# Performance work log

Hardware: AMD Instinct MI355X
Metric: run time of the kernel (lower is better)

## Reference

```python
import jax, jax.numpy as jnp
import numpy as np

D_MODEL = 768
NUM_HEADS = 12
D_K = D_MODEL // NUM_HEADS


def setup_inputs() -> dict:
    key = jax.random.key(0)
    ks = jax.random.split(key, 11)
    B, L = 1, 4096
    s = 1.0 / np.sqrt(D_MODEL)
    return {
        "q": jax.random.normal(ks[0], (B, L, D_MODEL), jnp.float32),
        "k": jax.random.normal(ks[1], (B, L, D_MODEL), jnp.float32),
        "v": jax.random.normal(ks[2], (B, L, D_MODEL), jnp.float32),
        "Wq": jax.random.normal(ks[3], (D_MODEL, D_MODEL), jnp.float32) * s,
        "bq": jax.random.normal(ks[4], (D_MODEL,), jnp.float32) * s,
        "Wk": jax.random.normal(ks[5], (D_MODEL, D_MODEL), jnp.float32) * s,
        "bk": jax.random.normal(ks[6], (D_MODEL,), jnp.float32) * s,
        "Wv": jax.random.normal(ks[7], (D_MODEL, D_MODEL), jnp.float32) * s,
        "bv": jax.random.normal(ks[8], (D_MODEL,), jnp.float32) * s,
        "Wo": jax.random.normal(ks[9], (D_MODEL, D_MODEL), jnp.float32) * s,
        "bo": jax.random.normal(ks[10], (D_MODEL,), jnp.float32) * s,
    }


def reference(q, k, v, Wq, bq, Wk, bk, Wv, bv, Wo, bo):
    B, L, _ = q.shape
    # linear projections (torch Linear: x @ W.T + b)
    qp = q @ Wq.T + bq
    kp = k @ Wk.T + bk
    vp = v @ Wv.T + bv
    # split heads: (B, H, L, d_k)
    def split(x):
        return x.reshape(B, L, NUM_HEADS, D_K).transpose(0, 2, 1, 3)
    qh, kh, vh = split(qp), split(kp), split(vp)
    scale = 1.0 / jnp.sqrt(jnp.asarray(D_K, qh.dtype))
    scores = jnp.einsum("bhqd,bhkd->bhqk", qh, kh) * scale  # (B,H,L,L)
    weights = jax.nn.softmax(scores, axis=-1)
    out = jnp.einsum("bhqk,bhkd->bhqd", weights, vh)
    out = out.transpose(0, 2, 1, 3).reshape(B, L, D_MODEL)
    return out @ Wo.T + bo
```

## Files before the change

### kernel.cpp

```cpp
#include <hip/hip_runtime.h>
#include <stdint.h>
#include <math.h>

#define L_SEQ  4096
#define DMODEL 768
#define NHEADS 12
#define DKH    64
#define QSCALE 0.18033688011112042f

typedef _Float16 f16;
typedef __attribute__((ext_vector_type(8))) _Float16 half8;
typedef __attribute__((ext_vector_type(4))) _Float16 half4;
typedef __attribute__((ext_vector_type(4))) float f32x4;
typedef __attribute__((ext_vector_type(16))) float f32x16;
typedef __attribute__((ext_vector_type(4))) unsigned int uint4v;

#define MFMA16(a, b, c) __builtin_amdgcn_mfma_f32_16x16x32_f16(a, b, c, 0, 0, 0)
#define MFMA32(a, b, c) __builtin_amdgcn_mfma_f32_32x32x16_f16(a, b, c, 0, 0, 0)

#define NE ((size_t)L_SEQ * DMODEL)
#define WE ((size_t)DMODEL * DMODEL)

static __device__ __forceinline__ unsigned int pack2(float a, float b) {
  return __builtin_bit_cast(unsigned int, __builtin_amdgcn_cvt_pkrtz(a, b));
}

__global__ __launch_bounds__(256)
void cvt_all(const float* __restrict__ q, const float* __restrict__ k,
             const float* __restrict__ v, const float* __restrict__ Wq,
             const float* __restrict__ Wk, const float* __restrict__ Wv,
             const float* __restrict__ Wo, f16* __restrict__ x16,
             f16* __restrict__ w16)
{
  const size_t NE4 = NE / 4, WE4 = WE / 4;
  size_t i = (size_t)blockIdx.x * 256 + threadIdx.x;
  const float* srcs[7] = {q, k, v, Wq, Wk, Wv, Wo};
  f16* dsts[7] = {x16, x16 + NE, x16 + 2 * NE,
                  w16, w16 + WE, w16 + 2 * WE, w16 + 3 * WE};
  const size_t sz4[7] = {NE4, NE4, NE4, WE4, WE4, WE4, WE4};
  int r = 0; size_t off = i;
  while (off >= sz4[r]) { off -= sz4[r]; ++r; }
  float4 f = reinterpret_cast<const float4*>(srcs[r])[off];
  half4 h; h[0] = (f16)f.x; h[1] = (f16)f.y; h[2] = (f16)f.z; h[3] = (f16)f.w;
  reinterpret_cast<half4*>(dsts[r])[off] = h;
}

#define GEMM_COMPUTE(acc)                                                     \
  { _Pragma("unroll")                                                         \
    for (int ks = 0; ks < 2; ++ks) {                                          \
      half8 bf[4];                                                            \
      _Pragma("unroll")                                                       \
      for (int nf = 0; nf < 4; ++nf)                                          \
        bf[nf] = *reinterpret_cast<half8*>(                                   \
            &Bs[wn + nf * 16 + lq][ks * 32 + quad * 8]);                      \
      _Pragma("unroll")                                                       \
      for (int mf = 0; mf < 4; ++mf) {                                        \
        half8 af = *reinterpret_cast<half8*>(                                 \
            &As[wm + mf * 16 + lq][ks * 32 + quad * 8]);                      \
        _Pragma("unroll")                                                     \
        for (int nf = 0; nf < 4; ++nf)                                        \
          acc[mf][nf] = MFMA16(af, bf[nf], acc[mf][nf]);                      \
      }                                                                       \
    } }

#define STAGE(aset, bset)                                                     \
  { _Pragma("unroll")                                                         \
    for (int u = 0; u < 4; ++u) {                                             \
      *reinterpret_cast<half8*>(&As[srow][sseg + u * 8]) = aset[u];           \
      *reinterpret_cast<half8*>(&Bs[srow][sseg + u * 8]) = bset[u];           \
    } }

#define GLOAD(aset, bset, t)                                                  \
  { _Pragma("unroll")                                                         \
    for (int u = 0; u < 4; ++u) {                                             \
      aset[u] = reinterpret_cast<const half8*>(aptr + (t) * 64)[u];           \
      bset[u] = reinterpret_cast<const half8*>(bptr + (t) * 64)[u];           \
    } }

__global__ __launch_bounds__(256)
void qkv_gemm(const f16* __restrict__ x16, const f16* __restrict__ w16,
              const float* __restrict__ bq, const float* __restrict__ bk,
              const float* __restrict__ bv,
              f16* __restrict__ Qp, f16* __restrict__ Kp, f16* __restrict__ VpT)
{
  __shared__ f16 As[128][72];
  __shared__ f16 Bs[128][72];
  const int tid  = threadIdx.x;
  const int lane = tid & 63, wid = tid >> 6;
  const int lq   = lane & 15, quad = lane >> 4;
  const int wm   = (wid & 1) * 64, wn = (wid >> 1) * 64;

  const int d   = blockIdx.x;
  const int r8  = d & 7;
  const int j   = d >> 3;
  const int g   = r8 + 8 * (j / 6);
  const int nb  = j % 6;
  const int widx = g / 32;
  const int m0   = (g % 32) * 128;
  const int n0   = nb * 128;

  const f16* X = x16 + (size_t)widx * NE;
  const f16* W = w16 + (size_t)widx * WE;
  const float* Bv = (widx == 0) ? bq : (widx == 1) ? bk : bv;

  const int srow = tid >> 1, sseg = (tid & 1) * 32;
  const f16* aptr = X + (size_t)(m0 + srow) * DMODEL + sseg;
  const f16* bptr = W + (size_t)(n0 + srow) * DMODEL + sseg;

  half8 aA[4], bA[4], aB[4], bB[4];
  GLOAD(aA, bA, 0);
  GLOAD(aB, bB, 1);

  f32x4 acc[4][4] = {};

  for (int it = 0; it < 12; it += 2) {
    STAGE(aA, bA);
    __syncthreads();
    if (it + 2 < 12) GLOAD(aA, bA, it + 2);
    GEMM_COMPUTE(acc);
    __syncthreads();

    STAGE(aB, bB);
    __syncthreads();
    if (it + 3 < 12) GLOAD(aB, bB, it + 3);
    GEMM_COMPUTE(acc);
    __syncthreads();
  }

#pragma unroll
  for (int nf = 0; nf < 4; ++nf) {
    const int col  = n0 + wn + nf * 16 + lq;
    const float bias = Bv[col];
#pragma unroll
    for (int mf = 0; mf < 4; ++mf) {
      const int rowb = m0 + wm + mf * 16 + quad * 4;
      if (widx == 2) {
        half4 o4;
#pragma unroll
        for (int r = 0; r < 4; ++r) o4[r] = (f16)(acc[mf][nf][r] + bias);
        *reinterpret_cast<half4*>(VpT + (size_t)col * L_SEQ + rowb) = o4;
      } else if (widx == 0) {
#pragma unroll
        for (int r = 0; r < 4; ++r)
          Qp[(size_t)(rowb + r) * DMODEL + col] = (f16)((acc[mf][nf][r] + bias) * QSCALE);
      } else {
#pragma unroll
        for (int r = 0; r < 4; ++r)
          Kp[(size_t)(rowb + r) * DMODEL + col] = (f16)(acc[mf][nf][r] + bias);
      }
    }
  }
}

__global__ __launch_bounds__(256, 3)
void attn_mfma4(const f16* __restrict__ Qp, const f16* __restrict__ Kp,
                const f16* __restrict__ VpT, f16* __restrict__ AO)
{
  const int h  = blockIdx.x;
  const int q0 = blockIdx.y * 64;
  const int tid  = threadIdx.x;
  const int lane = tid & 63, wid = tid >> 6;
  const int l31  = lane & 31, hc = lane >> 5;
  const int qh   = wid & 1, kh = wid >> 1;

  __shared__ __align__(16) char smem[36864];
  f16 (*Ks)[64][72] = (f16 (*)[64][72])smem;
  f16 (*Vt)[64][72] = (f16 (*)[64][72])(smem + 18432);
  float* Of  = (float*)smem;
  float* lf  = (float*)(smem + 16384);
  f16*   Of16 = (f16*)(smem + 16640);

  half8 qf[4];
#pragma unroll
  for (int st = 0; st < 4; ++st)
    qf[st] = *reinterpret_cast<const half8*>(
        Qp + (size_t)(q0 + qh * 32 + l31) * DMODEL + h * DKH + st * 16 + hc * 8);

  f32x16 oacc[2] = {};
  float lsum = 0.0f;

  const int srow = tid >> 2, sseg = (tid & 3) * 16;
  const f16* kbase = Kp  + (size_t)srow * DMODEL + h * DKH + sseg;
  const f16* vbase = VpT + (size_t)(h * DKH + srow) * L_SEQ + sseg;

  half8 k0 = *reinterpret_cast<const half8*>(kbase);
  half8 k1 = *reinterpret_cast<const half8*>(kbase + 8);
  half8 v0 = *reinterpret_cast<const half8*>(vbase);
  half8 v1 = *reinterpret_cast<const half8*>(vbase + 8);

  int p = 0;
  for (int kt = 0; kt < L_SEQ; kt += 64) {
    *reinterpret_cast<half8*>(&Ks[p][srow][sseg])     = k0;
    *reinterpret_cast<half8*>(&Ks[p][srow][sseg + 8]) = k1;
    *reinterpret_cast<half8*>(&Vt[p][srow][sseg])     = v0;
    *reinterpret_cast<half8*>(&Vt[p][srow][sseg + 8]) = v1;
    __syncthreads();

    if (kt + 64 < L_SEQ) {
      const f16* kn = kbase + (size_t)(kt + 64) * DMODEL;
      const f16* vn = vbase + (kt + 64);
      k0 = *reinterpret_cast<const half8*>(kn);
      k1 = *reinterpret_cast<const half8*>(kn + 8);
      v0 = *reinterpret_cast<const half8*>(vn);
      v1 = *reinterpret_cast<const half8*>(vn + 8);
    }

    __builtin_amdgcn_s_setprio(1);

    f32x16 s = {};
#pragma unroll
    for (int st = 0; st < 4; ++st) {
      half8 kf = *reinterpret_cast<half8*>(&Ks[p][kh * 32 + l31][st * 16 + hc * 8]);
      s = MFMA32(kf, qf[st], s);
    }

    unsigned int pk[8];
#pragma unroll
    for (int i = 0; i < 8; ++i) {
      float p0 = __builtin_amdgcn_exp2f(s[2 * i]);
      float p1 = __builtin_amdgcn_exp2f(s[2 * i + 1]);
      lsum += p0 + p1;
      pk[i] = pack2(p0, p1);
    }

#pragma unroll
    for (int st = 0; st < 2; ++st) {
      unsigned int w0 = pk[4 * st + 0], w1 = pk[4 * st + 1];
      unsigned int w2 = pk[4 * st + 2], w3 = pk[4 * st + 3];
      asm("v_permlane32_swap_b32 %0, %1" : "+v"(w0), "+v"(w2));
      asm("v_permlane32_swap_b32 %0, %1" : "+v"(w1), "+v"(w3));
      uint4v pw; pw[0] = w0; pw[1] = w1; pw[2] = w2; pw[3] = w3;
      half8 pf = __builtin_bit_cast(half8, pw);
#pragma unroll
      for (int a = 0; a < 2; ++a) {
        half8 vf = *reinterpret_cast<half8*>(&Vt[p][a * 32 + l31][kh * 32 + st * 16 + hc * 8]);
        oacc[a] = MFMA32(vf, pf, oacc[a]);
      }
    }
    __builtin_amdgcn_s_setprio(0);
    p ^= 1;
  }
  __syncthreads();

  float lw = lsum + __shfl_xor(lsum, 32);

  if (kh == 0) {
#pragma unroll
    for (int a = 0; a < 2; ++a)
#pragma unroll
      for (int r = 0; r < 16; ++r) {
        int d = a * 32 + (r & 3) + 8 * (r >> 2) + 4 * hc;
        Of[((qh * 64) + d) * 32 + l31] = oacc[a][r];
      }
    if (lane < 32) lf[qh * 32 + l31] = lw;
  }
  __syncthreads();
  if (kh == 1) {
    const float inv = 1.0f / (lf[qh * 32 + l31] + lw);
#pragma unroll
    for (int a = 0; a < 2; ++a)
#pragma unroll
      for (int r = 0; r < 16; ++r) {
        int d = a * 32 + (r & 3) + 8 * (r >> 2) + 4 * hc;
        float val = (Of[((qh * 64) + d) * 32 + l31] + oacc[a][r]) * inv;
        Of16[(qh * 32 + l31) * 64 + d] = (f16)val;
      }
  }
  __syncthreads();

  *reinterpret_cast<half8*>(AO + (size_t)(q0 + srow) * DMODEL + h * DKH + sseg) =
      *reinterpret_cast<half8*>(&Of16[srow * 64 + sseg]);
  *reinterpret_cast<half8*>(AO + (size_t)(q0 + srow) * DMODEL + h * DKH + sseg + 8) =
      *reinterpret_cast<half8*>(&Of16[srow * 64 + sseg + 8]);
}

__global__ __launch_bounds__(256)
void out_gemm(const f16* __restrict__ A, const f16* __restrict__ W,
              const float* __restrict__ Bv, float* __restrict__ O)
{
  __shared__ f16 As[128][72];
  __shared__ f16 Bs[128][72];
  const int tid  = threadIdx.x;
  const int lane = tid & 63, wid = tid >> 6;
  const int lq   = lane & 15, quad = lane >> 4;
  const int wm   = (wid & 1) * 64, wn = (wid >> 1) * 64;

  const int d   = blockIdx.x;
  const int r8  = d & 7;
  const int j   = d >> 3;
  const int g   = r8 + 8 * (j / 6);
  const int nb  = j % 6;
  const int m0  = g * 128, n0 = nb * 128;

  const int srow = tid >> 1, sseg = (tid & 1) * 32;
  const f16* aptr = A + (size_t)(m0 + srow) * DMODEL + sseg;
  const f16* bptr = W + (size_t)(n0 + srow) * DMODEL + sseg;

  half8 aA[4], bA[4], aB[4], bB[4];
  GLOAD(aA, bA, 0);
  GLOAD(aB, bB, 1);

  f32x4 acc[4][4] = {};

  for (int it = 0; it < 12; it += 2) {
    STAGE(aA, bA);
    __syncthreads();
    if (it + 2 < 12) GLOAD(aA, bA, it + 2);
    GEMM_COMPUTE(acc);
    __syncthreads();

    STAGE(aB, bB);
    __syncthreads();
    if (it + 3 < 12) GLOAD(aB, bB, it + 3);
    GEMM_COMPUTE(acc);
    __syncthreads();
  }

#pragma unroll
  for (int nf = 0; nf < 4; ++nf) {
    const int col = n0 + wn + nf * 16 + lq;
    const float bias = Bv[col];
#pragma unroll
    for (int mf = 0; mf < 4; ++mf) {
      const int rowb = m0 + wm + mf * 16 + quad * 4;
#pragma unroll
      for (int r = 0; r < 4; ++r)
        O[(size_t)(rowb + r) * DMODEL + col] = acc[mf][nf][r] + bias;
    }
  }
}

extern "C" void kernel_launch(void* const* d_in, const int* in_sizes, int n_in,
                              void* d_out, int out_size, void* d_ws, size_t ws_size,
                              hipStream_t stream) {
  const float* q  = (const float*)d_in[0];
  const float* k  = (const float*)d_in[1];
  const float* v  = (const float*)d_in[2];
  const float* Wq = (const float*)d_in[3];
  const float* bq = (const float*)d_in[4];
  const float* Wk = (const float*)d_in[5];
  const float* bk = (const float*)d_in[6];
  const float* Wv = (const float*)d_in[7];
  const float* bv = (const float*)d_in[8];
  const float* Wo = (const float*)d_in[9];
  const float* bo = (const float*)d_in[10];
  float* out = (float*)d_out;

  f16* x16 = (f16*)d_ws;
  f16* w16 = x16 + 3 * NE;
  f16* Qp  = w16 + 4 * WE;
  f16* Kp  = Qp + NE;
  f16* VpT = Kp + NE;
  f16* AO  = VpT + NE;

  const int ncvt = (int)((3 * (NE / 4) + 4 * (WE / 4)) / 256);
  cvt_all<<<ncvt, 256, 0, stream>>>(q, k, v, Wq, Wk, Wv, Wo, x16, w16);

  qkv_gemm<<<576, 256, 0, stream>>>(x16, w16, bq, bk, bv, Qp, Kp, VpT);

  dim3 gattn(NHEADS, L_SEQ / 64);
  attn_mfma4<<<gattn, 256, 0, stream>>>(Qp, Kp, VpT, AO);

  out_gemm<<<192, 256, 0, stream>>>(AO, w16 + 3 * WE, bo, out);
}
```

Measured before the change: 226.5 us.

## Widen attention blocks to 8 waves over 128-key tiles and halve QKV GEMM tile

```diff
diff --git a/kernel.cpp b/kernel.cpp
--- a/kernel.cpp
+++ b/kernel.cpp
@@ -45,6 +45,257 @@
   reinterpret_cast<half4*>(dsts[r])[off] = h;
 }
 
+#define QSTAGE(aset, bset)                                                    \
+  { _Pragma("unroll")                                                         \
+    for (int u = 0; u < 4; ++u)                                               \
+      *reinterpret_cast<half8*>(&As[arow][aseg + u * 8]) = aset[u];           \
+    _Pragma("unroll")                                                         \
+    for (int u = 0; u < 2; ++u)                                               \
+      *reinterpret_cast<half8*>(&Bs[brow][bseg + u * 8]) = bset[u];           \
+  }
+
+#define QGLOAD(aset, bset, t)                                                 \
+  { _Pragma("unroll")                                                         \
+    for (int u = 0; u < 4; ++u)                                               \
+      aset[u] = reinterpret_cast<const half8*>(aptr + (t) * 64)[u];           \
+    _Pragma("unroll")                                                         \
+    for (int u = 0; u < 2; ++u)                                               \
+      bset[u] = reinterpret_cast<const half8*>(bptr + (t) * 64)[u];           \
+  }
+
+#define QCOMPUTE(acc)                                                         \
+  { _Pragma("unroll")                                                         \
+    for (int ks = 0; ks < 2; ++ks) {                                          \
+      half8 bf[2];                                                            \
+      _Pragma("unroll")                                                       \
+      for (int nf = 0; nf < 2; ++nf)                                          \
+        bf[nf] = *reinterpret_cast<half8*>(                                   \
+            &Bs[wn + nf * 16 + lq][ks * 32 + quad * 8]);                      \
+      _Pragma("unroll")                                                       \
+      for (int mf = 0; mf < 4; ++mf) {                                        \
+        half8 af = *reinterpret_cast<half8*>(                                 \
+            &As[wm + mf * 16 + lq][ks * 32 + quad * 8]);                      \
+        _Pragma("unroll")                                                     \
+        for (int nf = 0; nf < 2; ++nf)                                        \
+          acc[mf][nf] = MFMA16(af, bf[nf], acc[mf][nf]);                      \
+      }                                                                       \
+    } }
+
+__global__ __launch_bounds__(256)
+void qkv_gemm(const f16* __restrict__ x16, const f16* __restrict__ w16,
+              const float* __restrict__ bq, const float* __restrict__ bk,
+              const float* __restrict__ bv,
+              f16* __restrict__ Qp, f16* __restrict__ Kp, f16* __restrict__ VpT)
+{
+  __shared__ f16 As[128][72];
+  __shared__ f16 Bs[64][72];
+  const int tid  = threadIdx.x;
+  const int lane = tid & 63, wid = tid >> 6;
+  const int lq   = lane & 15, quad = lane >> 4;
+  const int wm   = (wid & 1) * 64, wn = (wid >> 1) * 32;
+
+  const int d   = blockIdx.x;
+  const int r8  = d & 7;
+  const int j   = d >> 3;
+  const int g   = r8 + 8 * (j / 12);
+  const int nb  = j % 12;
+  const int widx = g / 32;
+  const int m0   = (g % 32) * 128;
+  const int n0   = nb * 64;
+
+  const f16* X = x16 + (size_t)widx * NE;
+  const f16* W = w16 + (size_t)widx * WE;
+  const float* Bv = (widx == 0) ? bq : (widx == 1) ? bk : bv;
+
+  const int arow = tid >> 1, aseg = (tid & 1) * 32;
+  const int brow = tid >> 2, bseg = (tid & 3) * 16;
+  const f16* aptr = X + (size_t)(m0 + arow) * DMODEL + aseg;
+  const f16* bptr = W + (size_t)(n0 + brow) * DMODEL + bseg;
+
+  half8 aA[4], bA[2], aB[4], bB[2];
+  QGLOAD(aA, bA, 0);
+  QGLOAD(aB, bB, 1);
+
+  f32x4 acc[4][2] = {};
+
+  for (int it = 0; it < 12; it += 2) {
+    QSTAGE(aA, bA);
+    __syncthreads();
+    if (it + 2 < 12) QGLOAD(aA, bA, it + 2);
+    QCOMPUTE(acc);
+    __syncthreads();
+
+    QSTAGE(aB, bB);
+    __syncthreads();
+    if (it + 3 < 12) QGLOAD(aB, bB, it + 3);
+    QCOMPUTE(acc);
+    __syncthreads();
+  }
+
+#pragma unroll
+  for (int nf = 0; nf < 2; ++nf) {
+    const int col  = n0 + wn + nf * 16 + lq;
+    const float bias = Bv[col];
+#pragma unroll
+    for (int mf = 0; mf < 4; ++mf) {
+      const int rowb = m0 + wm + mf * 16 + quad * 4;
+      if (widx == 2) {
+        half4 o4;
+#pragma unroll
+        for (int r = 0; r < 4; ++r) o4[r] = (f16)(acc[mf][nf][r] + bias);
+        *reinterpret_cast<half4*>(VpT + (size_t)col * L_SEQ + rowb) = o4;
+      } else if (widx == 0) {
+#pragma unroll
+        for (int r = 0; r < 4; ++r)
+          Qp[(size_t)(rowb + r) * DMODEL + col] = (f16)((acc[mf][nf][r] + bias) * QSCALE);
+      } else {
+#pragma unroll
+        for (int r = 0; r < 4; ++r)
+          Kp[(size_t)(rowb + r) * DMODEL + col] = (f16)(acc[mf][nf][r] + bias);
+      }
+    }
+  }
+}
+
+__global__ __launch_bounds__(512, 4)
+void attn_mfma4(const f16* __restrict__ Qp, const f16* __restrict__ Kp,
+                const f16* __restrict__ VpT, f16* __restrict__ AO)
+{
+  const int h  = blockIdx.x;
+  const int q0 = blockIdx.y * 64;
+  const int tid  = threadIdx.x;
+  const int lane = tid & 63, wid = tid >> 6;
+  const int l31  = lane & 31, hc = lane >> 5;
+  const int qh   = wid & 1;
+  const int kh   = (wid >> 1) & 1;
+  const int tt   = wid >> 2;
+  const int tb   = tt * 64;
+
+  __shared__ __align__(16) char smem[71680];
+  f16 (*Ks)[128][72]  = (f16 (*)[128][72])smem;
+  f16 (*Vt)[64][136]  = (f16 (*)[64][136])(smem + 36864);
+  float* Of  = (float*)smem;
+  float* lf  = (float*)(smem + 16384);
+  f16*   Of16 = (f16*)(smem + 16640);
+
+  half8 qf[4];
+#pragma unroll
+  for (int st = 0; st < 4; ++st)
+    qf[st] = *reinterpret_cast<const half8*>(
+        Qp + (size_t)(q0 + qh * 32 + l31) * DMODEL + h * DKH + st * 16 + hc * 8);
+
+  f32x16 oacc[2] = {};
+  float lsum = 0.0f;
+
+  const int krow = tid >> 2, kseg = (tid & 3) * 16;
+  const int vrow = tid >> 3, vseg = (tid & 7) * 16;
+  const f16* kbase = Kp  + (size_t)krow * DMODEL + h * DKH + kseg;
+  const f16* vbase = VpT + (size_t)(h * DKH + vrow) * L_SEQ + vseg;
+
+  half8 k0 = *reinterpret_cast<const half8*>(kbase);
+  half8 k1 = *reinterpret_cast<const half8*>(kbase + 8);
+  half8 v0 = *reinterpret_cast<const half8*>(vbase);
+  half8 v1 = *reinterpret_cast<const half8*>(vbase + 8);
+
+  int p = 0;
+  for (int kt = 0; kt < L_SEQ; kt += 128) {
+    *reinterpret_cast<half8*>(&Ks[p][krow][kseg])     = k0;
+    *reinterpret_cast<half8*>(&Ks[p][krow][kseg + 8]) = k1;
+    *reinterpret_cast<half8*>(&Vt[p][vrow][vseg])     = v0;
+    *reinterpret_cast<half8*>(&Vt[p][vrow][vseg + 8]) = v1;
+    __syncthreads();
+
+    if (kt + 128 < L_SEQ) {
+      const f16* kn = kbase + (size_t)(kt + 128) * DMODEL;
+      const f16* vn = vbase + (kt + 128);
+      k0 = *reinterpret_cast<const half8*>(kn);
+      k1 = *reinterpret_cast<const half8*>(kn + 8);
+      v0 = *reinterpret_cast<const half8*>(vn);
+      v1 = *reinterpret_cast<const half8*>(vn + 8);
+    }
+
+    __builtin_amdgcn_s_setprio(1);
+
+    f32x16 s = {};
+#pragma unroll
+    for (int st = 0; st < 4; ++st) {
+      half8 kf = *reinterpret_cast<half8*>(&Ks[p][tb + kh * 32 + l31][st * 16 + hc * 8]);
+      s = MFMA32(kf, qf[st], s);
+    }
+
+    unsigned int pk[8];
+#pragma unroll
+    for (int i = 0; i < 8; ++i) {
+      float p0 = __builtin_amdgcn_exp2f(s[2 * i]);
+      float p1 = __builtin_amdgcn_exp2f(s[2 * i + 1]);
+      lsum += p0 + p1;
+      pk[i] = pack2(p0, p1);
+    }
+
+#pragma unroll
+    for (int st = 0; st < 2; ++st) {
+      unsigned int w0 = pk[4 * st + 0], w1 = pk[4 * st + 1];
+      unsigned int w2 = pk[4 * st + 2], w3 = pk[4 * st + 3];
+      asm("v_permlane32_swap_b32 %0, %1" : "+v"(w0), "+v"(w2));
+      asm("v_permlane32_swap_b32 %0, %1" : "+v"(w1), "+v"(w3));
+      uint4v pw; pw[0] = w0; pw[1] = w1; pw[2] = w2; pw[3] = w3;
+      half8 pf = __builtin_bit_cast(half8, pw);
+#pragma unroll
+      for (int a = 0; a < 2; ++a) {
+        half8 vf = *reinterpret_cast<half8*>(
+            &Vt[p][a * 32 + l31][tb + kh * 32 + st * 16 + hc * 8]);
+        oacc[a] = MFMA32(vf, pf, oacc[a]);
+      }
+    }
+    __builtin_amdgcn_s_setprio(0);
+    p ^= 1;
+  }
+  __syncthreads();
+
+  const float lw = lsum + __shfl_xor(lsum, 32);
+  const int pid = kh + 2 * tt;
+
+#pragma unroll
+  for (int rnd = 0; rnd < 4; ++rnd) {
+    if (pid == rnd) {
+      if (rnd == 0) {
+#pragma unroll
+        for (int a = 0; a < 2; ++a)
+#pragma unroll
+          for (int r = 0; r < 16; ++r) {
+            int dd = a * 32 + (r & 3) + 8 * (r >> 2) + 4 * hc;
+            Of[((qh * 64) + dd) * 32 + l31] = oacc[a][r];
+          }
+        if (lane < 32) lf[qh * 32 + l31] = lw;
+      } else if (rnd < 3) {
+#pragma unroll
+        for (int a = 0; a < 2; ++a)
+#pragma unroll
+          for (int r = 0; r < 16; ++r) {
+            int dd = a * 32 + (r & 3) + 8 * (r >> 2) + 4 * hc;
+            Of[((qh * 64) + dd) * 32 + l31] += oacc[a][r];
+          }
+        if (lane < 32) lf[qh * 32 + l31] += lw;
+      } else {
+        const float inv = 1.0f / (lf[qh * 32 + l31] + lw);
+#pragma unroll
+        for (int a = 0; a < 2; ++a)
+#pragma unroll
+          for (int r = 0; r < 16; ++r) {
+            int dd = a * 32 + (r & 3) + 8 * (r >> 2) + 4 * hc;
+            float val = (Of[((qh * 64) + dd) * 32 + l31] + oacc[a][r]) * inv;
+            Of16[(qh * 32 + l31) * 64 + dd] = (f16)val;
+          }
+      }
+    }
+    __syncthreads();
+  }
+
+  const int orow = tid >> 3, oseg = (tid & 7) * 8;
+  *reinterpret_cast<half8*>(AO + (size_t)(q0 + orow) * DMODEL + h * DKH + oseg) =
+      *reinterpret_cast<half8*>(&Of16[orow * 64 + oseg]);
+}
+
 #define GEMM_COMPUTE(acc)                                                     \
   { _Pragma("unroll")                                                         \
     for (int ks = 0; ks < 2; ++ks) {                                          \
@@ -78,203 +329,6 @@
     } }
 
 __global__ __launch_bounds__(256)
-void qkv_gemm(const f16* __restrict__ x16, const f16* __restrict__ w16,
-              const float* __restrict__ bq, const float* __restrict__ bk,
-              const float* __restrict__ bv,
-              f16* __restrict__ Qp, f16* __restrict__ Kp, f16* __restrict__ VpT)
-{
-  __shared__ f16 As[128][72];
-  __shared__ f16 Bs[128][72];
-  const int tid  = threadIdx.x;
-  const int lane = tid & 63, wid = tid >> 6;
-  const int lq   = lane & 15, quad = lane >> 4;
-  const int wm   = (wid & 1) * 64, wn = (wid >> 1) * 64;
-
-  const int d   = blockIdx.x;
-  const int r8  = d & 7;
-  const int j   = d >> 3;
-  const int g   = r8 + 8 * (j / 6);
-  const int nb  = j % 6;
-  const int widx = g / 32;
-  const int m0   = (g % 32) * 128;
-  const int n0   = nb * 128;
-
-  const f16* X = x16 + (size_t)widx * NE;
-  const f16* W = w16 + (size_t)widx * WE;
-  const float* Bv = (widx == 0) ? bq : (widx == 1) ? bk : bv;
-
-  const int srow = tid >> 1, sseg = (tid & 1) * 32;
-  const f16* aptr = X + (size_t)(m0 + srow) * DMODEL + sseg;
-  const f16* bptr = W + (size_t)(n0 + srow) * DMODEL + sseg;
-
-  half8 aA[4], bA[4], aB[4], bB[4];
-  GLOAD(aA, bA, 0);
-  GLOAD(aB, bB, 1);
-
-  f32x4 acc[4][4] = {};
-
-  for (int it = 0; it < 12; it += 2) {
-    STAGE(aA, bA);
-    __syncthreads();
-    if (it + 2 < 12) GLOAD(aA, bA, it + 2);
-    GEMM_COMPUTE(acc);
-    __syncthreads();
-
-    STAGE(aB, bB);
-    __syncthreads();
-    if (it + 3 < 12) GLOAD(aB, bB, it + 3);
-    GEMM_COMPUTE(acc);
-    __syncthreads();
-  }
-
-#pragma unroll
-  for (int nf = 0; nf < 4; ++nf) {
-    const int col  = n0 + wn + nf * 16 + lq;
-    const float bias = Bv[col];
-#pragma unroll
-    for (int mf = 0; mf < 4; ++mf) {
-      const int rowb = m0 + wm + mf * 16 + quad * 4;
-      if (widx == 2) {
-        half4 o4;
-#pragma unroll
-        for (int r = 0; r < 4; ++r) o4[r] = (f16)(acc[mf][nf][r] + bias);
-        *reinterpret_cast<half4*>(VpT + (size_t)col * L_SEQ + rowb) = o4;
-      } else if (widx == 0) {
-#pragma unroll
-        for (int r = 0; r < 4; ++r)
-          Qp[(size_t)(rowb + r) * DMODEL + col] = (f16)((acc[mf][nf][r] + bias) * QSCALE);
-      } else {
-#pragma unroll
-        for (int r = 0; r < 4; ++r)
-          Kp[(size_t)(rowb + r) * DMODEL + col] = (f16)(acc[mf][nf][r] + bias);
-      }
-    }
-  }
-}
-
-__global__ __launch_bounds__(256, 3)
-void attn_mfma4(const f16* __restrict__ Qp, const f16* __restrict__ Kp,
-                const f16* __restrict__ VpT, f16* __restrict__ AO)
-{
-  const int h  = blockIdx.x;
-  const int q0 = blockIdx.y * 64;
-  const int tid  = threadIdx.x;
-  const int lane = tid & 63, wid = tid >> 6;
-  const int l31  = lane & 31, hc = lane >> 5;
-  const int qh   = wid & 1, kh = wid >> 1;
-
-  __shared__ __align__(16) char smem[36864];
-  f16 (*Ks)[64][72] = (f16 (*)[64][72])smem;
-  f16 (*Vt)[64][72] = (f16 (*)[64][72])(smem + 18432);
-  float* Of  = (float*)smem;
-  float* lf  = (float*)(smem + 16384);
-  f16*   Of16 = (f16*)(smem + 16640);
-
-  half8 qf[4];
-#pragma unroll
-  for (int st = 0; st < 4; ++st)
-    qf[st] = *reinterpret_cast<const half8*>(
-        Qp + (size_t)(q0 + qh * 32 + l31) * DMODEL + h * DKH + st * 16 + hc * 8);
-
-  f32x16 oacc[2] = {};
-  float lsum = 0.0f;
-
-  const int srow = tid >> 2, sseg = (tid & 3) * 16;
-  const f16* kbase = Kp  + (size_t)srow * DMODEL + h * DKH + sseg;
-  const f16* vbase = VpT + (size_t)(h * DKH + srow) * L_SEQ + sseg;
-
-  half8 k0 = *reinterpret_cast<const half8*>(kbase);
-  half8 k1 = *reinterpret_cast<const half8*>(kbase + 8);
-  half8 v0 = *reinterpret_cast<const half8*>(vbase);
-  half8 v1 = *reinterpret_cast<const half8*>(vbase + 8);
-
-  int p = 0;
-  for (int kt = 0; kt < L_SEQ; kt += 64) {
-    *reinterpret_cast<half8*>(&Ks[p][srow][sseg])     = k0;
-    *reinterpret_cast<half8*>(&Ks[p][srow][sseg + 8]) = k1;
-    *reinterpret_cast<half8*>(&Vt[p][srow][sseg])     = v0;
-    *reinterpret_cast<half8*>(&Vt[p][srow][sseg + 8]) = v1;
-    __syncthreads();
-
-    if (kt + 64 < L_SEQ) {
-      const f16* kn = kbase + (size_t)(kt + 64) * DMODEL;
-      const f16* vn = vbase + (kt + 64);
-      k0 = *reinterpret_cast<const half8*>(kn);
-      k1 = *reinterpret_cast<const half8*>(kn + 8);
-      v0 = *reinterpret_cast<const half8*>(vn);
-      v1 = *reinterpret_cast<const half8*>(vn + 8);
-    }
-
-    __builtin_amdgcn_s_setprio(1);
-
-    f32x16 s = {};
-#pragma unroll
-    for (int st = 0; st < 4; ++st) {
-      half8 kf = *reinterpret_cast<half8*>(&Ks[p][kh * 32 + l31][st * 16 + hc * 8]);
-      s = MFMA32(kf, qf[st], s);
-    }
-
-    unsigned int pk[8];
-#pragma unroll
-    for (int i = 0; i < 8; ++i) {
-      float p0 = __builtin_amdgcn_exp2f(s[2 * i]);
-      float p1 = __builtin_amdgcn_exp2f(s[2 * i + 1]);
-      lsum += p0 + p1;
-      pk[i] = pack2(p0, p1);
-    }
-
-#pragma unroll
-    for (int st = 0; st < 2; ++st) {
-      unsigned int w0 = pk[4 * st + 0], w1 = pk[4 * st + 1];
-      unsigned int w2 = pk[4 * st + 2], w3 = pk[4 * st + 3];
-      asm("v_permlane32_swap_b32 %0, %1" : "+v"(w0), "+v"(w2));
-      asm("v_permlane32_swap_b32 %0, %1" : "+v"(w1), "+v"(w3));
-      uint4v pw; pw[0] = w0; pw[1] = w1; pw[2] = w2; pw[3] = w3;
-      half8 pf = __builtin_bit_cast(half8, pw);
-#pragma unroll
-      for (int a = 0; a < 2; ++a) {
-        half8 vf = *reinterpret_cast<half8*>(&Vt[p][a * 32 + l31][kh * 32 + st * 16 + hc * 8]);
-        oacc[a] = MFMA32(vf, pf, oacc[a]);
-      }
-    }
-    __builtin_amdgcn_s_setprio(0);
-    p ^= 1;
-  }
-  __syncthreads();
-
-  float lw = lsum + __shfl_xor(lsum, 32);
-
-  if (kh == 0) {
-#pragma unroll
-    for (int a = 0; a < 2; ++a)
-#pragma unroll
-      for (int r = 0; r < 16; ++r) {
-        int d = a * 32 + (r & 3) + 8 * (r >> 2) + 4 * hc;
-        Of[((qh * 64) + d) * 32 + l31] = oacc[a][r];
-      }
-    if (lane < 32) lf[qh * 32 + l31] = lw;
-  }
-  __syncthreads();
-  if (kh == 1) {
-    const float inv = 1.0f / (lf[qh * 32 + l31] + lw);
-#pragma unroll
-    for (int a = 0; a < 2; ++a)
-#pragma unroll
-      for (int r = 0; r < 16; ++r) {
-        int d = a * 32 + (r & 3) + 8 * (r >> 2) + 4 * hc;
-        float val = (Of[((qh * 64) + d) * 32 + l31] + oacc[a][r]) * inv;
-        Of16[(qh * 32 + l31) * 64 + d] = (f16)val;
-      }
-  }
-  __syncthreads();
-
-  *reinterpret_cast<half8*>(AO + (size_t)(q0 + srow) * DMODEL + h * DKH + sseg) =
-      *reinterpret_cast<half8*>(&Of16[srow * 64 + sseg]);
-  *reinterpret_cast<half8*>(AO + (size_t)(q0 + srow) * DMODEL + h * DKH + sseg + 8) =
-      *reinterpret_cast<half8*>(&Of16[srow * 64 + sseg + 8]);
-}
-
-__global__ __launch_bounds__(256)
 void out_gemm(const f16* __restrict__ A, const f16* __restrict__ W,
               const float* __restrict__ Bv, float* __restrict__ O)
 {
@@ -356,10 +410,10 @@
   const int ncvt = (int)((3 * (NE / 4) + 4 * (WE / 4)) / 256);
   cvt_all<<<ncvt, 256, 0, stream>>>(q, k, v, Wq, Wk, Wv, Wo, x16, w16);
 
-  qkv_gemm<<<576, 256, 0, stream>>>(x16, w16, bq, bk, bv, Qp, Kp, VpT);
+  qkv_gemm<<<1152, 256, 0, stream>>>(x16, w16, bq, bk, bv, Qp, Kp, VpT);
 
   dim3 gattn(NHEADS, L_SEQ / 64);
-  attn_mfma4<<<gattn, 256, 0, stream>>>(Qp, Kp, VpT, AO);
+  attn_mfma4<<<gattn, 512, 0, stream>>>(Qp, Kp, VpT, AO);
 
   out_gemm<<<192, 256, 0, stream>>>(AO, w16 + 3 * WE, bo, out);
 }
```

Result: faster. 220.5 us (-2.7%).
